# Optimization experiments

Measured on AMD Instinct MI355X. Metric: run time of the kernel, lower is better.

## Reference

```python
import jax, jax.numpy as jnp
import numpy as np
from math import sqrt

T_TEMP = 1.0  # softmax temperature (init arg T)
NEG_INF = -1e30  # finite stand-in for -inf; masked probs are exactly 0 after softmax


def setup_inputs() -> dict:
    key = jax.random.key(0)
    kq, kk, kv = jax.random.split(key, 3)
    B, L, H, E = 4, 2048, 16, 64
    queries = jax.random.normal(kq, (B, L, H, E), dtype=jnp.float32)
    keys = jax.random.normal(kk, (B, L, H, E), dtype=jnp.float32)
    values = jax.random.normal(kv, (B, L, H, E), dtype=jnp.float32)
    return {"queries": queries, "keys": keys, "values": values}


def reference(queries, keys, values):
    # queries: [B,L,H,E], keys: [B,S,H,E], values: [B,S,H,D]
    B, L, H, E = queries.shape
    S = keys.shape[1]
    scale = 1.0 / sqrt(E)
    # scores: [B,H,L,S]
    scores = jnp.einsum('blhe,bshe->bhls', queries, keys) * scale
    # causal mask: True above diagonal -> masked out (TriangularCausalMask)
    causal = jnp.triu(jnp.ones((L, S), dtype=bool), k=1)
    scores = jnp.where(causal, NEG_INF, scores)
    A = jax.nn.softmax(scores / T_TEMP, axis=-1)  # dropout p=0 -> identity
    V = jnp.einsum('bhls,bshd->blhd', A, values)
    return V
```

## Files before the change

kernel.cpp:

```cpp
#include <hip/hip_runtime.h>


typedef __attribute__((ext_vector_type(8))) unsigned short u16x8;
typedef __attribute__((ext_vector_type(4))) unsigned short u16x4;
typedef __attribute__((ext_vector_type(8))) __bf16 bf16x8;
typedef __attribute__((ext_vector_type(4))) float f32x4;

#define LOG2E 1.44269504088896340736f
#define AS1 __attribute__((address_space(1)))
#define AS3 __attribute__((address_space(3)))

static __device__ __forceinline__ unsigned short f32_bf16_rne(float x) {
    unsigned int b = __builtin_bit_cast(unsigned int, x);
    b = (b + 0x7fffu + ((b >> 16) & 1u)) >> 16;
    return (unsigned short)b;
}

static __device__ __forceinline__ int swzs(int row) {
    return (row & 6) | ((row >> 3) & 1);
}
static __device__ __forceinline__ int tileIdx(int row, int col) {
    return row * 64 + (((col >> 3) ^ swzs(row)) << 3) + (col & 7);
}

__global__ __launch_bounds__(256) void prep_kernel(
    const float* __restrict__ K, const float* __restrict__ V,
    unsigned short* __restrict__ wsK, unsigned short* __restrict__ wsV)
{
    const int ROW = 1024;
    const int tid = threadIdx.x;
    const int kt  = blockIdx.x;
    const int bh  = blockIdx.y;
    const size_t tileBase = (size_t)(bh >> 4) * 2048 * ROW + (size_t)(bh & 15) * 64
                          + (size_t)(kt * 64) * ROW;
    unsigned short* kimg = wsK + (((size_t)bh * 32 + kt) << 12);
    unsigned short* vimg = wsV + (((size_t)bh * 32 + kt) << 12);

    const int kRow = tid >> 4, kCol = (tid & 15) * 4;
    #pragma unroll
    for (int j = 0; j < 4; ++j) {
        const int key = j * 16 + kRow;
        f32x4 v = *(const f32x4*)(K + tileBase + (size_t)key * ROW + kCol);
        u16x4 w;
        #pragma unroll
        for (int i = 0; i < 4; ++i) w[i] = f32_bf16_rne(v[i]);
        *(u16x4*)&kimg[tileIdx(key, kCol)] = w;
    }
    const int vKey2 = (tid & 31) * 2, vDbase = (tid >> 5) * 8;
    const float* r0 = V + tileBase + (size_t)vKey2 * ROW + vDbase;
    #pragma unroll
    for (int j = 0; j < 2; ++j) {
        f32x4 va = *(const f32x4*)(r0 + j * 4);
        f32x4 vb = *(const f32x4*)(r0 + ROW + j * 4);
        #pragma unroll
        for (int i = 0; i < 4; ++i) {
            unsigned int pk = (unsigned int)f32_bf16_rne(va[i])
                            | ((unsigned int)f32_bf16_rne(vb[i]) << 16);
            *(unsigned int*)&vimg[tileIdx(vDbase + j * 4 + i, vKey2)] = pk;
        }
    }
}

__global__ __launch_bounds__(256, 4) void fattn2_kernel(
    const float* __restrict__ Q,
    const unsigned short* __restrict__ wsK,
    const unsigned short* __restrict__ wsV,
    float* __restrict__ O)
{
    const int ROW = 1024;

    const int tid  = threadIdx.x;
    const int wave = tid >> 6;
    const int lane = tid & 63;
    const int quad = lane >> 4;
    const int n16  = lane & 15;

    const int id   = blockIdx.x;
    const int k8   = id & 7;
    const int rest = id >> 3;
    const int bh   = k8 * 8 + (rest >> 4);
    const int xb   = rest & 15;
    const size_t headBase = (size_t)(bh >> 4) * 2048 * ROW + (size_t)(bh & 15) * 64;

    __shared__ __align__(16) unsigned short sK[2][4096];
    __shared__ __align__(16) unsigned short sV[2][4096];
    __shared__ __align__(16) unsigned short sP[4][1024];

    int kvIdx[4];
    #pragma unroll
    for (int nb = 0; nb < 4; ++nb) {
        const int row = nb * 16 + n16;
        kvIdx[nb] = row * 64 + ((quad ^ swzs(row)) << 3);
    }
    const int pIdx = n16 * 64 + ((quad ^ swzs(n16)) << 3);

    const float c0 = 0.125f * LOG2E;

    for (int qi = 0; qi < 2; ++qi) {
        const int qtile = qi ? (31 - xb) : xb;
        const int q0 = qtile * 64 + wave * 16;

        bf16x8 qf0, qf1;
        {
            const float* qrow = Q + headBase + (size_t)(q0 + n16) * ROW + quad * 8;
            u16x8 a, b;
            #pragma unroll
            for (int i = 0; i < 8; ++i) {
                a[i] = f32_bf16_rne(qrow[i] * c0);
                b[i] = f32_bf16_rne(qrow[32 + i] * c0);
            }
            qf0 = __builtin_bit_cast(bf16x8, a);
            qf1 = __builtin_bit_cast(bf16x8, b);
        }

        f32x4 oacc[4];
        #pragma unroll
        for (int d = 0; d < 4; ++d) oacc[d] = (f32x4){0.f, 0.f, 0.f, 0.f};
        float l_r[4];
        #pragma unroll
        for (int r = 0; r < 4; ++r) l_r[r] = 0.f;

        const int nT = qtile + 1;

        #define STAGE(buf, kt_)                                                   \
        do {                                                                      \
            const size_t toff = (((size_t)bh * 32 + (kt_)) << 12);                \
            const unsigned short* kg = wsK + toff + wave * 1024 + lane * 8;       \
            const unsigned short* vg = wsV + toff + wave * 1024 + lane * 8;       \
            __builtin_amdgcn_global_load_lds((const AS1 unsigned int*)kg,         \
                (AS3 unsigned int*)&sK[buf][wave * 1024], 16, 0, 0);              \
            __builtin_amdgcn_global_load_lds((const AS1 unsigned int*)(kg + 512), \
                (AS3 unsigned int*)&sK[buf][wave * 1024 + 512], 16, 0, 0);        \
            __builtin_amdgcn_global_load_lds((const AS1 unsigned int*)vg,         \
                (AS3 unsigned int*)&sV[buf][wave * 1024], 16, 0, 0);              \
            __builtin_amdgcn_global_load_lds((const AS1 unsigned int*)(vg + 512), \
                (AS3 unsigned int*)&sV[buf][wave * 1024 + 512], 16, 0, 0);        \
        } while (0)

        __syncthreads();
        STAGE(0, 0);

        for (int kt = 0; kt < nT; ++kt) {
            const int cur = kt & 1;

            __syncthreads();

            if (kt + 1 < nT) STAGE(cur ^ 1, kt + 1);

            f32x4 sacc[4];
            #pragma unroll
            for (int nb = 0; nb < 4; ++nb) {
                bf16x8 b0 = __builtin_bit_cast(bf16x8, *(const u16x8*)&sK[cur][kvIdx[nb]]);
                bf16x8 b1 = __builtin_bit_cast(bf16x8, *(const u16x8*)&sK[cur][kvIdx[nb] ^ 32]);
                f32x4 s = (f32x4){0.f, 0.f, 0.f, 0.f};
                s = __builtin_amdgcn_mfma_f32_16x16x32_bf16(qf0, b0, s, 0, 0, 0);
                s = __builtin_amdgcn_mfma_f32_16x16x32_bf16(qf1, b1, s, 0, 0, 0);
                sacc[nb] = s;
            }

            if (kt == qtile) {
                #pragma unroll
                for (int nb = 0; nb < 4; ++nb) {
                    const int keyl = nb * 16 + n16;
                    #pragma unroll
                    for (int r = 0; r < 4; ++r) {
                        const int ql = wave * 16 + quad * 4 + r;
                        sacc[nb][r] = (keyl > ql) ? -1e30f : sacc[nb][r];
                    }
                }
            }

            #pragma unroll
            for (int r = 0; r < 4; ++r) {
                const int qrl = quad * 4 + r;
                const int pwBase = qrl * 64 + (n16 & 7);
                const int sw = swzs(qrl);
                const int hb = n16 >> 3;
                float ps = 0.f;
                #pragma unroll
                for (int nb = 0; nb < 4; ++nb) {
                    unsigned short u = f32_bf16_rne(__builtin_amdgcn_exp2f(sacc[nb][r]));
                    ps += __builtin_bit_cast(float, (unsigned int)u << 16);
                    sP[wave][pwBase + (((nb * 2 + hb) ^ sw) << 3)] = u;
                }
                l_r[r] += ps;
            }

            #pragma unroll
            for (int kh = 0; kh < 2; ++kh) {
                bf16x8 ap = __builtin_bit_cast(bf16x8,
                    *(const u16x8*)&sP[wave][pIdx ^ (kh << 5)]);
                #pragma unroll
                for (int d = 0; d < 4; ++d) {
                    bf16x8 vf = __builtin_bit_cast(bf16x8,
                        *(const u16x8*)&sV[cur][kvIdx[d] ^ (kh << 5)]);
                    oacc[d] = __builtin_amdgcn_mfma_f32_16x16x32_bf16(ap, vf, oacc[d], 0, 0, 0);
                }
            }
        }
        #undef STAGE

        float inv[4];
        #pragma unroll
        for (int r = 0; r < 4; ++r) {
            float l = l_r[r];
            #pragma unroll
            for (int off = 1; off < 16; off <<= 1)
                l += __shfl_xor(l, off, 64);
            inv[r] = 1.0f / l;
        }
        #pragma unroll
        for (int d = 0; d < 4; ++d) {
            #pragma unroll
            for (int r = 0; r < 4; ++r) {
                const int qg = q0 + quad * 4 + r;
                O[headBase + (size_t)qg * ROW + d * 16 + n16] = oacc[d][r] * inv[r];
            }
        }
    }
}

__global__ __launch_bounds__(256, 4) void fattn_kernel(
    const float* __restrict__ Q,
    const float* __restrict__ K,
    const float* __restrict__ V,
    float* __restrict__ O)
{
    const int ROW = 1024;
    const int tid  = threadIdx.x;
    const int wave = tid >> 6;
    const int lane = tid & 63;
    const int quad = lane >> 4;
    const int n16  = lane & 15;
    const int xb = blockIdx.x;
    const int bh = blockIdx.y;
    const size_t headBase = (size_t)(bh >> 4) * 2048 * ROW + (size_t)(bh & 15) * 64;

    __shared__ __align__(16) unsigned short sK[4096];
    __shared__ __align__(16) unsigned short sV[4096];
    __shared__ __align__(16) unsigned short sP[4][1024];

    int kvIdx[4];
    #pragma unroll
    for (int nb = 0; nb < 4; ++nb) {
        const int row = nb * 16 + n16;
        kvIdx[nb] = row * 64 + ((quad ^ swzs(row)) << 3);
    }
    const int pIdx = n16 * 64 + ((quad ^ swzs(n16)) << 3);
    const int kStageRow = tid >> 4;
    const int kStageCol = (tid & 15) * 4;
    const int vKey2  = (tid & 31) * 2;
    const int vDbase = (tid >> 5) * 8;
    const float c0 = 0.125f * LOG2E;

    for (int qi = 0; qi < 2; ++qi) {
        const int qtile = qi ? (31 - xb) : xb;
        const int q0 = qtile * 64 + wave * 16;
        bf16x8 qf0, qf1;
        {
            const float* qrow = Q + headBase + (size_t)(q0 + n16) * ROW + quad * 8;
            u16x8 a, b;
            #pragma unroll
            for (int i = 0; i < 8; ++i) {
                a[i] = f32_bf16_rne(qrow[i] * c0);
                b[i] = f32_bf16_rne(qrow[32 + i] * c0);
            }
            qf0 = __builtin_bit_cast(bf16x8, a);
            qf1 = __builtin_bit_cast(bf16x8, b);
        }
        f32x4 oacc[4];
        #pragma unroll
        for (int d = 0; d < 4; ++d) oacc[d] = (f32x4){0.f, 0.f, 0.f, 0.f};
        float l_r[4];
        #pragma unroll
        for (int r = 0; r < 4; ++r) l_r[r] = 0.f;
        const int nT = qtile + 1;
        f32x4 pk[4], pva[2], pvb[2];
        {
            const float* kb = K + headBase;
            const float* r0 = V + headBase + (size_t)vKey2 * ROW + vDbase;
            #pragma unroll
            for (int j = 0; j < 4; ++j)
                pk[j] = *(const f32x4*)(kb + (size_t)(j * 16 + kStageRow) * ROW + kStageCol);
            #pragma unroll
            for (int j = 0; j < 2; ++j) {
                pva[j] = *(const f32x4*)(r0 + j * 4);
                pvb[j] = *(const f32x4*)(r0 + ROW + j * 4);
            }
        }
        for (int kt = 0; kt < nT; ++kt) {
            __syncthreads();
            #pragma unroll
            for (int j = 0; j < 4; ++j) {
                u16x4 w;
                #pragma unroll
                for (int i = 0; i < 4; ++i) w[i] = f32_bf16_rne(pk[j][i]);
                *(u16x4*)&sK[tileIdx(j * 16 + kStageRow, kStageCol)] = w;
            }
            #pragma unroll
            for (int j = 0; j < 2; ++j) {
                const int d0 = vDbase + j * 4;
                #pragma unroll
                for (int i = 0; i < 4; ++i) {
                    unsigned int pkk = (unsigned int)f32_bf16_rne(pva[j][i])
                                     | ((unsigned int)f32_bf16_rne(pvb[j][i]) << 16);
                    *(unsigned int*)&sV[tileIdx(d0 + i, vKey2)] = pkk;
                }
            }
            if (kt + 1 < nT) {
                const size_t nb2 = headBase + (size_t)((kt + 1) * 64) * ROW;
                const float* kb = K + nb2;
                const float* r0 = V + nb2 + (size_t)vKey2 * ROW + vDbase;
                #pragma unroll
                for (int j = 0; j < 4; ++j)
                    pk[j] = *(const f32x4*)(kb + (size_t)(j * 16 + kStageRow) * ROW + kStageCol);
                #pragma unroll
                for (int j = 0; j < 2; ++j) {
                    pva[j] = *(const f32x4*)(r0 + j * 4);
                    pvb[j] = *(const f32x4*)(r0 + ROW + j * 4);
                }
            }
            __syncthreads();
            f32x4 sacc[4];
            #pragma unroll
            for (int nb = 0; nb < 4; ++nb) {
                bf16x8 b0 = __builtin_bit_cast(bf16x8, *(const u16x8*)&sK[kvIdx[nb]]);
                bf16x8 b1 = __builtin_bit_cast(bf16x8, *(const u16x8*)&sK[kvIdx[nb] ^ 32]);
                f32x4 s = (f32x4){0.f, 0.f, 0.f, 0.f};
                s = __builtin_amdgcn_mfma_f32_16x16x32_bf16(qf0, b0, s, 0, 0, 0);
                s = __builtin_amdgcn_mfma_f32_16x16x32_bf16(qf1, b1, s, 0, 0, 0);
                sacc[nb] = s;
            }
            if (kt == qtile) {
                #pragma unroll
                for (int nb = 0; nb < 4; ++nb) {
                    const int keyl = nb * 16 + n16;
                    #pragma unroll
                    for (int r = 0; r < 4; ++r) {
                        const int ql = wave * 16 + quad * 4 + r;
                        sacc[nb][r] = (keyl > ql) ? -1e30f : sacc[nb][r];
                    }
                }
            }
            #pragma unroll
            for (int r = 0; r < 4; ++r) {
                const int qrl = quad * 4 + r;
                const int pwBase = qrl * 64 + (n16 & 7);
                const int sw = swzs(qrl);
                const int hb = n16 >> 3;
                float ps = 0.f;
                #pragma unroll
                for (int nb = 0; nb < 4; ++nb) {
                    unsigned short u = f32_bf16_rne(__builtin_amdgcn_exp2f(sacc[nb][r]));
                    ps += __builtin_bit_cast(float, (unsigned int)u << 16);
                    sP[wave][pwBase + (((nb * 2 + hb) ^ sw) << 3)] = u;
                }
                l_r[r] += ps;
            }
            #pragma unroll
            for (int kh = 0; kh < 2; ++kh) {
                bf16x8 ap = __builtin_bit_cast(bf16x8,
                    *(const u16x8*)&sP[wave][pIdx ^ (kh << 5)]);
                #pragma unroll
                for (int d = 0; d < 4; ++d) {
                    bf16x8 vf = __builtin_bit_cast(bf16x8,
                        *(const u16x8*)&sV[kvIdx[d] ^ (kh << 5)]);
                    oacc[d] = __builtin_amdgcn_mfma_f32_16x16x32_bf16(ap, vf, oacc[d], 0, 0, 0);
                }
            }
        }
        float inv[4];
        #pragma unroll
        for (int r = 0; r < 4; ++r) {
            float l = l_r[r];
            #pragma unroll
            for (int off = 1; off < 16; off <<= 1)
                l += __shfl_xor(l, off, 64);
            inv[r] = 1.0f / l;
        }
        #pragma unroll
        for (int d = 0; d < 4; ++d) {
            #pragma unroll
            for (int r = 0; r < 4; ++r) {
                const int qg = q0 + quad * 4 + r;
                O[headBase + (size_t)qg * ROW + d * 16 + n16] = oacc[d][r] * inv[r];
            }
        }
    }
}

extern "C" void kernel_launch(void* const* d_in, const int* in_sizes, int n_in,
                              void* d_out, int out_size, void* d_ws, size_t ws_size,
                              hipStream_t stream) {
    const float* Q = (const float*)d_in[0];
    const float* K = (const float*)d_in[1];
    const float* V = (const float*)d_in[2];
    float* Out = (float*)d_out;

    const size_t imgElems = (size_t)64 * 32 * 4096;
    if (ws_size >= imgElems * 2 * sizeof(unsigned short)) {
        unsigned short* wsK = (unsigned short*)d_ws;
        unsigned short* wsV = wsK + imgElems;
        hipLaunchKernelGGL(prep_kernel, dim3(32, 64), dim3(256), 0, stream, K, V, wsK, wsV);
        hipLaunchKernelGGL(fattn2_kernel, dim3(1024), dim3(256), 0, stream, Q, wsK, wsV, Out);
    } else {
        hipLaunchKernelGGL(fattn_kernel, dim3(16, 64), dim3(256), 0, stream, Q, K, V, Out);
    }
}
```

Before: 200.1 us.

## Rework flash attention to 32x32 MFMA tiles with register P exchange

The main attention kernel now uses 32x32x16 bf16 MFMAs with 2 waves per block, each wave handling 32 query rows. It computes S transposed so the probabilities can be passed between lane halves with shuffles, removing the shared-memory round trip for P. The grid changes to one block per query tile ordered from longest to shortest, and the output is staged through LDS for coalesced vector stores. The prep kernel is rewritten to build the K and V bf16 images through LDS with a packed convert instruction. The new K/V tile layouts and the causal masking must match the new MFMA fragment mappings exactly.

```diff
diff --git a/kernel.cpp b/kernel.cpp
--- a/kernel.cpp
+++ b/kernel.cpp
@@ -5,6 +5,8 @@
 typedef __attribute__((ext_vector_type(4))) unsigned short u16x4;
 typedef __attribute__((ext_vector_type(8))) __bf16 bf16x8;
 typedef __attribute__((ext_vector_type(4))) float f32x4;
+typedef __attribute__((ext_vector_type(16))) float f32x16;
+typedef __attribute__((ext_vector_type(4))) unsigned int u32x4;
 
 #define LOG2E 1.44269504088896340736f
 #define AS1 __attribute__((address_space(1)))
@@ -14,6 +16,12 @@
     unsigned int b = __builtin_bit_cast(unsigned int, x);
     b = (b + 0x7fffu + ((b >> 16) & 1u)) >> 16;
     return (unsigned short)b;
+}
+
+static __device__ __forceinline__ unsigned int cvt_pk_bf16(float lo, float hi) {
+    unsigned int r;
+    asm("v_cvt_pk_bf16_f32 %0, %1, %2" : "=v"(r) : "v"(lo), "v"(hi));
+    return r;
 }
 
 static __device__ __forceinline__ int swzs(int row) {
@@ -36,32 +44,67 @@
     unsigned short* kimg = wsK + (((size_t)bh * 32 + kt) << 12);
     unsigned short* vimg = wsV + (((size_t)bh * 32 + kt) << 12);
 
-    const int kRow = tid >> 4, kCol = (tid & 15) * 4;
-    #pragma unroll
-    for (int j = 0; j < 4; ++j) {
-        const int key = j * 16 + kRow;
-        f32x4 v = *(const f32x4*)(K + tileBase + (size_t)key * ROW + kCol);
-        u16x4 w;
-        #pragma unroll
-        for (int i = 0; i < 4; ++i) w[i] = f32_bf16_rne(v[i]);
-        *(u16x4*)&kimg[tileIdx(key, kCol)] = w;
-    }
-    const int vKey2 = (tid & 31) * 2, vDbase = (tid >> 5) * 8;
-    const float* r0 = V + tileBase + (size_t)vKey2 * ROW + vDbase;
-    #pragma unroll
-    for (int j = 0; j < 2; ++j) {
-        f32x4 va = *(const f32x4*)(r0 + j * 4);
-        f32x4 vb = *(const f32x4*)(r0 + ROW + j * 4);
+    __shared__ __align__(16) unsigned short ik[4096];
+    __shared__ unsigned int sT[64 * 33];
+
+    {
+        const int key = tid & 63, ec = tid >> 6;
+        const float* kr = K + tileBase + (size_t)key * ROW + ec * 16;
         #pragma unroll
         for (int i = 0; i < 4; ++i) {
-            unsigned int pk = (unsigned int)f32_bf16_rne(va[i])
-                            | ((unsigned int)f32_bf16_rne(vb[i]) << 16);
-            *(unsigned int*)&vimg[tileIdx(vDbase + j * 4 + i, vKey2)] = pk;
-        }
-    }
-}
-
-__global__ __launch_bounds__(256, 4) void fattn2_kernel(
+            f32x4 v = *(const f32x4*)(kr + 4 * i);
+            u16x4 w;
+            #pragma unroll
+            for (int j = 0; j < 4; ++j) w[j] = f32_bf16_rne(v[j]);
+            const int e = ec * 16 + 4 * i;
+            *(u16x4*)&ik[(e >> 3) * 512 + key * 8 + (e & 7)] = w;
+        }
+    }
+
+    {
+        const int kp = tid & 31, d0 = (tid >> 5) * 8;
+        const float* v0 = V + tileBase + (size_t)(2 * kp) * ROW + d0;
+        f32x4 a0 = *(const f32x4*)(v0);
+        f32x4 a1 = *(const f32x4*)(v0 + 4);
+        f32x4 b0 = *(const f32x4*)(v0 + ROW);
+        f32x4 b1 = *(const f32x4*)(v0 + ROW + 4);
+        #pragma unroll
+        for (int i = 0; i < 4; ++i) {
+            sT[(d0 + i) * 33 + kp]     = cvt_pk_bf16(a0[i], b0[i]);
+            sT[(d0 + 4 + i) * 33 + kp] = cvt_pk_bf16(a1[i], b1[i]);
+        }
+    }
+    __syncthreads();
+
+    {
+        const u32x4* src = (const u32x4*)ik;
+        u32x4* dst = (u32x4*)kimg;
+        dst[tid]       = src[tid];
+        dst[256 + tid] = src[256 + tid];
+    }
+    {
+        u32x4* vd = (u32x4*)vimg;
+        u32x4 w0, w1;
+        #pragma unroll
+        for (int j = 0; j < 4; ++j) {
+            const int unit = tid;
+            const int kc8 = unit >> 6, dx = unit & 63;
+            const int d = dx ^ kc8, kp = kc8 * 4 + j;
+            w0[j] = sT[d * 33 + kp];
+        }
+        #pragma unroll
+        for (int j = 0; j < 4; ++j) {
+            const int unit = 256 + tid;
+            const int kc8 = unit >> 6, dx = unit & 63;
+            const int d = dx ^ kc8, kp = kc8 * 4 + j;
+            w1[j] = sT[d * 33 + kp];
+        }
+        vd[tid]       = w0;
+        vd[256 + tid] = w1;
+    }
+}
+
+__global__ __launch_bounds__(128, 4) void fattn2_kernel(
     const float* __restrict__ Q,
     const unsigned short* __restrict__ wsK,
     const unsigned short* __restrict__ wsV,
@@ -72,151 +115,171 @@
     const int tid  = threadIdx.x;
     const int wave = tid >> 6;
     const int lane = tid & 63;
-    const int quad = lane >> 4;
-    const int n16  = lane & 15;
-
-    const int id   = blockIdx.x;
-    const int k8   = id & 7;
-    const int rest = id >> 3;
-    const int bh   = k8 * 8 + (rest >> 4);
-    const int xb   = rest & 15;
+    const int s    = lane >> 5;
+    const int n32  = lane & 31;
+    const bool hi32 = (s != 0);
+
+    const int id    = blockIdx.x;
+    const int qtile = 31 - (id >> 6);
+    const int bh    = id & 63;
     const size_t headBase = (size_t)(bh >> 4) * 2048 * ROW + (size_t)(bh & 15) * 64;
+    const int q0 = qtile * 64 + wave * 32;
 
     __shared__ __align__(16) unsigned short sK[2][4096];
     __shared__ __align__(16) unsigned short sV[2][4096];
-    __shared__ __align__(16) unsigned short sP[4][1024];
-
-    int kvIdx[4];
+
+    const int kbase = s * 1024 + n32 * 16;
+    int vbase[4];
     #pragma unroll
-    for (int nb = 0; nb < 4; ++nb) {
-        const int row = nb * 16 + n16;
-        kvIdx[nb] = row * 64 + ((quad ^ swzs(row)) << 3);
-    }
-    const int pIdx = n16 * 64 + ((quad ^ swzs(n16)) << 3);
+    for (int c = 0; c < 4; ++c)
+        vbase[c] = c * 2048 + s * 1024 + ((n32 ^ (2 * c + s)) << 4);
 
     const float c0 = 0.125f * LOG2E;
 
-    for (int qi = 0; qi < 2; ++qi) {
-        const int qtile = qi ? (31 - xb) : xb;
-        const int q0 = qtile * 64 + wave * 16;
-
-        bf16x8 qf0, qf1;
-        {
-            const float* qrow = Q + headBase + (size_t)(q0 + n16) * ROW + quad * 8;
-            u16x8 a, b;
-            #pragma unroll
-            for (int i = 0; i < 8; ++i) {
-                a[i] = f32_bf16_rne(qrow[i] * c0);
-                b[i] = f32_bf16_rne(qrow[32 + i] * c0);
-            }
-            qf0 = __builtin_bit_cast(bf16x8, a);
-            qf1 = __builtin_bit_cast(bf16x8, b);
-        }
-
-        f32x4 oacc[4];
-        #pragma unroll
-        for (int d = 0; d < 4; ++d) oacc[d] = (f32x4){0.f, 0.f, 0.f, 0.f};
-        float l_r[4];
-        #pragma unroll
-        for (int r = 0; r < 4; ++r) l_r[r] = 0.f;
-
-        const int nT = qtile + 1;
-
-        #define STAGE(buf, kt_)                                                   \
-        do {                                                                      \
-            const size_t toff = (((size_t)bh * 32 + (kt_)) << 12);                \
-            const unsigned short* kg = wsK + toff + wave * 1024 + lane * 8;       \
-            const unsigned short* vg = wsV + toff + wave * 1024 + lane * 8;       \
-            __builtin_amdgcn_global_load_lds((const AS1 unsigned int*)kg,         \
-                (AS3 unsigned int*)&sK[buf][wave * 1024], 16, 0, 0);              \
-            __builtin_amdgcn_global_load_lds((const AS1 unsigned int*)(kg + 512), \
-                (AS3 unsigned int*)&sK[buf][wave * 1024 + 512], 16, 0, 0);        \
-            __builtin_amdgcn_global_load_lds((const AS1 unsigned int*)vg,         \
-                (AS3 unsigned int*)&sV[buf][wave * 1024], 16, 0, 0);              \
-            __builtin_amdgcn_global_load_lds((const AS1 unsigned int*)(vg + 512), \
-                (AS3 unsigned int*)&sV[buf][wave * 1024 + 512], 16, 0, 0);        \
+    bf16x8 qf[4];
+    {
+        const float* qrow = Q + headBase + (size_t)(q0 + n32) * ROW + s * 8;
+        #pragma unroll
+        for (int c = 0; c < 4; ++c) {
+            f32x4 v0 = *(const f32x4*)(qrow + 16 * c);
+            f32x4 v1 = *(const f32x4*)(qrow + 16 * c + 4);
+            u32x4 a;
+            a[0] = cvt_pk_bf16(v0[0] * c0, v0[1] * c0);
+            a[1] = cvt_pk_bf16(v0[2] * c0, v0[3] * c0);
+            a[2] = cvt_pk_bf16(v1[0] * c0, v1[1] * c0);
+            a[3] = cvt_pk_bf16(v1[2] * c0, v1[3] * c0);
+            qf[c] = __builtin_bit_cast(bf16x8, a);
+        }
+    }
+
+    f32x16 oacc0, oacc1;
+    #pragma unroll
+    for (int r = 0; r < 16; ++r) { oacc0[r] = 0.f; oacc1[r] = 0.f; }
+    float l = 0.f;
+
+    const int nT = qtile + 1;
+
+    #define STAGE(buf, kt_)                                                    \
+    do {                                                                       \
+        const size_t toff = (((size_t)bh * 32 + (kt_)) << 12);                 \
+        const unsigned short* kg = wsK + toff + wave * 2048 + lane * 8;        \
+        const unsigned short* vg = wsV + toff + wave * 2048 + lane * 8;        \
+        __builtin_amdgcn_global_load_lds((const AS1 unsigned int*)kg,          \
+            (AS3 unsigned int*)&sK[buf][wave * 2048], 16, 0, 0);               \
+        __builtin_amdgcn_global_load_lds((const AS1 unsigned int*)(kg + 512),  \
+            (AS3 unsigned int*)&sK[buf][wave * 2048 + 512], 16, 0, 0);         \
+        __builtin_amdgcn_global_load_lds((const AS1 unsigned int*)(kg + 1024), \
+            (AS3 unsigned int*)&sK[buf][wave * 2048 + 1024], 16, 0, 0);        \
+        __builtin_amdgcn_global_load_lds((const AS1 unsigned int*)(kg + 1536), \
+            (AS3 unsigned int*)&sK[buf][wave * 2048 + 1536], 16, 0, 0);        \
+        __builtin_amdgcn_global_load_lds((const AS1 unsigned int*)vg,          \
+            (AS3 unsigned int*)&sV[buf][wave * 2048], 16, 0, 0);               \
+        __builtin_amdgcn_global_load_lds((const AS1 unsigned int*)(vg + 512),  \
+            (AS3 unsigned int*)&sV[buf][wave * 2048 + 512], 16, 0, 0);         \
+        __builtin_amdgcn_global_load_lds((const AS1 unsigned int*)(vg + 1024), \
+            (AS3 unsigned int*)&sV[buf][wave * 2048 + 1024], 16, 0, 0);        \
+        __builtin_amdgcn_global_load_lds((const AS1 unsigned int*)(vg + 1536), \
+            (AS3 unsigned int*)&sV[buf][wave * 2048 + 1536], 16, 0, 0);        \
+    } while (0)
+
+    STAGE(0, 0);
+
+    for (int kt = 0; kt < nT; ++kt) {
+        const int cur = kt & 1;
+
+        __syncthreads();
+
+        if (kt + 1 < nT) STAGE(cur ^ 1, kt + 1);
+
+        const char* kb = (const char*)&sK[cur][0];
+        const char* vb = (const char*)&sV[cur][0];
+
+        f32x16 s0v, s1v;
+        #pragma unroll
+        for (int r = 0; r < 16; ++r) { s0v[r] = 0.f; s1v[r] = 0.f; }
+        #pragma unroll
+        for (int c = 0; c < 4; ++c) {
+            bf16x8 k0 = __builtin_bit_cast(bf16x8,
+                *(const u16x8*)(kb + kbase + c * 2048));
+            bf16x8 k1 = __builtin_bit_cast(bf16x8,
+                *(const u16x8*)(kb + kbase + c * 2048 + 512));
+            s0v = __builtin_amdgcn_mfma_f32_32x32x16_bf16(k0, qf[c], s0v, 0, 0, 0);
+            s1v = __builtin_amdgcn_mfma_f32_32x32x16_bf16(k1, qf[c], s1v, 0, 0, 0);
+        }
+
+        if (kt == qtile) {
+            const int ql = wave * 32 + n32;
+            #pragma unroll
+            for (int r = 0; r < 16; ++r) {
+                const int k0 = (r & 3) + 8 * (r >> 2) + 4 * s;
+                s0v[r] = (k0 > ql) ? -1e30f : s0v[r];
+                s1v[r] = (k0 + 32 > ql) ? -1e30f : s1v[r];
+            }
+        }
+
+        float la = 0.f, lb = 0.f;
+        #pragma unroll
+        for (int r = 0; r < 16; ++r) {
+            s0v[r] = __builtin_amdgcn_exp2f(s0v[r]);
+            s1v[r] = __builtin_amdgcn_exp2f(s1v[r]);
+            la += s0v[r];
+            lb += s1v[r];
+        }
+        l += la + lb;
+
+        bf16x8 bp[4];
+        #define XCHG(pe, cc, DST)                                              \
+        do {                                                                   \
+            unsigned int P0 = cvt_pk_bf16(pe[8*(cc)+0], pe[8*(cc)+1]);         \
+            unsigned int P1 = cvt_pk_bf16(pe[8*(cc)+2], pe[8*(cc)+3]);         \
+            unsigned int P2 = cvt_pk_bf16(pe[8*(cc)+4], pe[8*(cc)+5]);         \
+            unsigned int P3 = cvt_pk_bf16(pe[8*(cc)+6], pe[8*(cc)+7]);         \
+            unsigned int x0 = __shfl_xor(P0, 32, 64);                          \
+            unsigned int x1 = __shfl_xor(P1, 32, 64);                          \
+            unsigned int x2 = __shfl_xor(P2, 32, 64);                          \
+            unsigned int x3 = __shfl_xor(P3, 32, 64);                          \
+            u32x4 bw;                                                          \
+            bw[0] = hi32 ? x2 : P0;                                            \
+            bw[1] = hi32 ? x3 : P1;                                            \
+            bw[2] = hi32 ? P2 : x0;                                            \
+            bw[3] = hi32 ? P3 : x1;                                            \
+            DST = __builtin_bit_cast(bf16x8, bw);                              \
         } while (0)
-
-        __syncthreads();
-        STAGE(0, 0);
-
-        for (int kt = 0; kt < nT; ++kt) {
-            const int cur = kt & 1;
-
-            __syncthreads();
-
-            if (kt + 1 < nT) STAGE(cur ^ 1, kt + 1);
-
-            f32x4 sacc[4];
-            #pragma unroll
-            for (int nb = 0; nb < 4; ++nb) {
-                bf16x8 b0 = __builtin_bit_cast(bf16x8, *(const u16x8*)&sK[cur][kvIdx[nb]]);
-                bf16x8 b1 = __builtin_bit_cast(bf16x8, *(const u16x8*)&sK[cur][kvIdx[nb] ^ 32]);
-                f32x4 s = (f32x4){0.f, 0.f, 0.f, 0.f};
-                s = __builtin_amdgcn_mfma_f32_16x16x32_bf16(qf0, b0, s, 0, 0, 0);
-                s = __builtin_amdgcn_mfma_f32_16x16x32_bf16(qf1, b1, s, 0, 0, 0);
-                sacc[nb] = s;
-            }
-
-            if (kt == qtile) {
-                #pragma unroll
-                for (int nb = 0; nb < 4; ++nb) {
-                    const int keyl = nb * 16 + n16;
-                    #pragma unroll
-                    for (int r = 0; r < 4; ++r) {
-                        const int ql = wave * 16 + quad * 4 + r;
-                        sacc[nb][r] = (keyl > ql) ? -1e30f : sacc[nb][r];
-                    }
-                }
-            }
-
-            #pragma unroll
-            for (int r = 0; r < 4; ++r) {
-                const int qrl = quad * 4 + r;
-                const int pwBase = qrl * 64 + (n16 & 7);
-                const int sw = swzs(qrl);
-                const int hb = n16 >> 3;
-                float ps = 0.f;
-                #pragma unroll
-                for (int nb = 0; nb < 4; ++nb) {
-                    unsigned short u = f32_bf16_rne(__builtin_amdgcn_exp2f(sacc[nb][r]));
-                    ps += __builtin_bit_cast(float, (unsigned int)u << 16);
-                    sP[wave][pwBase + (((nb * 2 + hb) ^ sw) << 3)] = u;
-                }
-                l_r[r] += ps;
-            }
-
-            #pragma unroll
-            for (int kh = 0; kh < 2; ++kh) {
-                bf16x8 ap = __builtin_bit_cast(bf16x8,
-                    *(const u16x8*)&sP[wave][pIdx ^ (kh << 5)]);
-                #pragma unroll
-                for (int d = 0; d < 4; ++d) {
-                    bf16x8 vf = __builtin_bit_cast(bf16x8,
-                        *(const u16x8*)&sV[cur][kvIdx[d] ^ (kh << 5)]);
-                    oacc[d] = __builtin_amdgcn_mfma_f32_16x16x32_bf16(ap, vf, oacc[d], 0, 0, 0);
-                }
-            }
-        }
-        #undef STAGE
-
-        float inv[4];
-        #pragma unroll
-        for (int r = 0; r < 4; ++r) {
-            float l = l_r[r];
-            #pragma unroll
-            for (int off = 1; off < 16; off <<= 1)
-                l += __shfl_xor(l, off, 64);
-            inv[r] = 1.0f / l;
-        }
-        #pragma unroll
-        for (int d = 0; d < 4; ++d) {
-            #pragma unroll
-            for (int r = 0; r < 4; ++r) {
-                const int qg = q0 + quad * 4 + r;
-                O[headBase + (size_t)qg * ROW + d * 16 + n16] = oacc[d][r] * inv[r];
-            }
-        }
+        XCHG(s0v, 0, bp[0]);
+        XCHG(s0v, 1, bp[1]);
+        XCHG(s1v, 0, bp[2]);
+        XCHG(s1v, 1, bp[3]);
+        #undef XCHG
+
+        #pragma unroll
+        for (int c = 0; c < 4; ++c) {
+            bf16x8 v0 = __builtin_bit_cast(bf16x8,
+                *(const u16x8*)(vb + vbase[c]));
+            bf16x8 v1 = __builtin_bit_cast(bf16x8,
+                *(const u16x8*)(vb + vbase[c] + 512));
+            oacc0 = __builtin_amdgcn_mfma_f32_32x32x16_bf16(v0, bp[c], oacc0, 0, 0, 0);
+            oacc1 = __builtin_amdgcn_mfma_f32_32x32x16_bf16(v1, bp[c], oacc1, 0, 0, 0);
+        }
+    }
+    #undef STAGE
+
+    l += __shfl_xor(l, 32, 64);
+    const float inv = 1.0f / l;
+
+    __syncthreads();
+    float* tb = wave ? (float*)&sV[0][0] : (float*)&sK[0][0];
+    #pragma unroll
+    for (int r = 0; r < 16; ++r) {
+        const int d0 = (r & 3) + 8 * (r >> 2) + 4 * s;
+        tb[n32 * 68 + d0]      = oacc0[r] * inv;
+        tb[n32 * 68 + d0 + 32] = oacc1[r] * inv;
+    }
+    #pragma unroll
+    for (int it = 0; it < 8; ++it) {
+        const int row = (lane >> 2) + 16 * (it & 1);
+        const int c4  = (lane & 3) + 4 * (it >> 1);
+        f32x4 v = *(const f32x4*)&tb[row * 68 + c4 * 4];
+        *(f32x4*)&O[headBase + (size_t)(q0 + row) * ROW + c4 * 4] = v;
     }
 }
 
@@ -326,10 +389,10 @@
             for (int nb = 0; nb < 4; ++nb) {
                 bf16x8 b0 = __builtin_bit_cast(bf16x8, *(const u16x8*)&sK[kvIdx[nb]]);
                 bf16x8 b1 = __builtin_bit_cast(bf16x8, *(const u16x8*)&sK[kvIdx[nb] ^ 32]);
-                f32x4 s = (f32x4){0.f, 0.f, 0.f, 0.f};
-                s = __builtin_amdgcn_mfma_f32_16x16x32_bf16(qf0, b0, s, 0, 0, 0);
-                s = __builtin_amdgcn_mfma_f32_16x16x32_bf16(qf1, b1, s, 0, 0, 0);
-                sacc[nb] = s;
+                f32x4 ss = (f32x4){0.f, 0.f, 0.f, 0.f};
+                ss = __builtin_amdgcn_mfma_f32_16x16x32_bf16(qf0, b0, ss, 0, 0, 0);
+                ss = __builtin_amdgcn_mfma_f32_16x16x32_bf16(qf1, b1, ss, 0, 0, 0);
+                sacc[nb] = ss;
             }
             if (kt == qtile) {
                 #pragma unroll
@@ -402,7 +465,7 @@
         unsigned short* wsK = (unsigned short*)d_ws;
         unsigned short* wsV = wsK + imgElems;
         hipLaunchKernelGGL(prep_kernel, dim3(32, 64), dim3(256), 0, stream, K, V, wsK, wsV);
-        hipLaunchKernelGGL(fattn2_kernel, dim3(1024), dim3(256), 0, stream, Q, wsK, wsV, Out);
+        hipLaunchKernelGGL(fattn2_kernel, dim3(2048), dim3(128), 0, stream, Q, wsK, wsV, Out);
     } else {
         hipLaunchKernelGGL(fattn_kernel, dim3(16, 64), dim3(256), 0, stream, Q, K, V, Out);
     }
```

New measurement: 197.8 us. Within noise of the previous version (-1.2%).
